# Performance work log

Measured on AMD Instinct MI355X. Metric: run time of the kernel, lower is better.

The kernel has to match this reference:

```python
import jax, jax.numpy as jnp
import numpy as np

SNUM = 8           # number of select-PUF stages
PUF_LEN = 64       # arbiter PUF length -> phi dim = PUF_LEN + 1
BATCH = 262144     # number of challenge-response pairs
D = 2 ** SNUM      # 256 combinations


def _make_kron_tables():
    """Replicates the W/B kron construction from combineMPUF.__init__.
    Returns Wmat, Bmat of shape [SNUM, D]; row i is W[i]/B[i] (originally [1, D])."""
    tmpX = np.array([[1], [1]])
    Ws, Bs = [], []
    for i in range(SNUM):
        w = np.array([[-1], [1]])
        b = np.array([[1], [0]])
        for _ in range(i + 1, SNUM):
            w = np.kron(tmpX, w)
            b = np.kron(tmpX, b)
        for _ in range(i):
            w = np.kron(w, tmpX)
            b = np.kron(b, tmpX)
        Ws.append(w.T[0])
        Bs.append(b.T[0])
    return (jnp.asarray(np.stack(Ws), jnp.float32),
            jnp.asarray(np.stack(Bs), jnp.float32))


def setup_inputs() -> dict:
    key = jax.random.key(0)
    k_phi, k_ws, k_bs, k_wd, k_bd = jax.random.split(key, 5)
    F = PUF_LEN + 1
    scale = 1.0 / np.sqrt(F)  # ~ torch Linear init scale
    phi = jax.random.normal(k_phi, (BATCH, F), dtype=jnp.float32)
    W_S = jax.random.uniform(k_ws, (SNUM, F), jnp.float32, -scale, scale)
    b_S = jax.random.uniform(k_bs, (SNUM,), jnp.float32, -scale, scale)
    W_D = jax.random.uniform(k_wd, (D, F), jnp.float32, -scale, scale)
    b_D = jax.random.uniform(k_bd, (D,), jnp.float32, -scale, scale)
    Wmat, Bmat = _make_kron_tables()
    return {"phi": phi, "W_S": W_S, "b_S": b_S, "W_D": W_D, "b_D": b_D,
            "Wmat": Wmat, "Bmat": Bmat}


def reference(phi, W_S, b_S, W_D, b_D, Wmat, Bmat):
    # phi: [B, F]; W_S: [SNUM, F]; W_D: [D, F]; Wmat/Bmat: [SNUM, D]
    Sdelta = phi @ W_S.T + b_S            # [B, SNUM]
    Ddelta = phi @ W_D.T + b_D            # [B, D]
    Souts = jax.nn.sigmoid(Sdelta)        # [B, SNUM]
    Douts = jax.nn.sigmoid(Ddelta)        # [B, D]
    # sigmoid-gated outer-product chain: M = prod_i (s_i * w_i + b_i)
    M = jnp.ones_like(Douts)
    for i in range(SNUM):                 # small fixed structural loop
        M = M * (Souts[:, i:i + 1] * Wmat[i] + Bmat[i])
    ans = jnp.sum(Douts * M * 0.99999, axis=-1, keepdims=True)  # [B, 1]
    reliability_output = jnp.abs(Sdelta)  # [B, SNUM]
    return ans, reliability_output
```

## Files before the change

### kernel.cpp

```cpp
#include <hip/hip_runtime.h>

typedef float  f32x4  __attribute__((ext_vector_type(4)));
typedef float  f32x4a __attribute__((ext_vector_type(4), aligned(4)));
typedef float  f32x2a __attribute__((ext_vector_type(2), aligned(4)));
typedef __bf16 bf16x8 __attribute__((ext_vector_type(8)));
typedef short  short8 __attribute__((ext_vector_type(8)));

#define F      65
#define NTT    17
#define KS3    3
#define RPB    128
#define NCHUNK (NTT*KS3*64)
#define NEGL2E -1.4426950408889634f

__device__ __forceinline__ float fast_sigmoid(float x) {
  float e = __builtin_amdgcn_exp2f(NEGL2E * x);
  return __builtin_amdgcn_rcpf(1.0f + e);
}
__device__ __forceinline__ float sig_prescaled(float a) {
  return __builtin_amdgcn_rcpf(1.0f + __builtin_amdgcn_exp2f(a));
}
template<int CTRL>
__device__ __forceinline__ float dpp_mov(float v) {
  return __builtin_bit_cast(float,
    __builtin_amdgcn_update_dpp(0, __builtin_bit_cast(int, v), CTRL, 0xF, 0xF, true));
}
__device__ __forceinline__ float reduce16(float v) {
  v += dpp_mov<0xB1>(v);
  v += dpp_mov<0x4E>(v);
  v += dpp_mov<0x141>(v);
  v += dpp_mov<0x140>(v);
  return v;
}

__global__ void prep_w(const float* __restrict__ W_S, const float* __restrict__ b_S,
                       const float* __restrict__ W_D, const float* __restrict__ b_D,
                       unsigned short* __restrict__ wsb) {
  int b = blockIdx.x;
  int t = b / 3, s = b % 3;
  int l = threadIdx.x;
  int c = l & 15, q = l >> 4;
  short8 out;
#pragma unroll
  for (int j = 0; j < 8; ++j) {
    int k = 32 * s + 8 * q + j;
    float v = 0.0f;
    if (t < 16) {
      int n = 16 * t + c;
      if (k < F)       v = NEGL2E * W_D[n * F + k];
      else if (k == F) v = NEGL2E * b_D[n];
    } else if (c < 8) {
      if (k < F)       v = W_S[c * F + k];
      else if (k == F) v = b_S[c];
    }
    unsigned int u = __builtin_bit_cast(unsigned int, v);
    u += 0x7FFFu + ((u >> 16) & 1u);
    out[j] = (short)(u >> 16);
  }
  reinterpret_cast<short8*>(wsb)[b * 64 + l] = out;
}

__launch_bounds__(256, 2)
__global__ void mpuf_main(const float* __restrict__ phi,
                          const unsigned short* __restrict__ wsb,
                          float* __restrict__ out_ans,
                          float* __restrict__ out_rel) {
  __shared__ short8 ldsB[NCHUNK];
  __shared__ float  soutv[RPB][9];
  __shared__ float  mtrec[RPB][20];

  const int tid  = threadIdx.x;
  const int wave = tid >> 6;
  const int l    = tid & 63;
  const int c    = l & 15;
  const int q    = l >> 4;
  const int wrow = wave * 32;
  const int brow = blockIdx.x * RPB;

  const float* prow0 = phi + (size_t)(brow + wrow + c) * F;
  const float* prow1 = prow0 + (size_t)16 * F;

  f32x4a f40[4], f41[4];
#pragma unroll
  for (int s = 0; s < 2; ++s) {
    f40[2 * s]     = *reinterpret_cast<const f32x4a*>(prow0 + 32 * s + 8 * q);
    f40[2 * s + 1] = *reinterpret_cast<const f32x4a*>(prow0 + 32 * s + 8 * q + 4);
    f41[2 * s]     = *reinterpret_cast<const f32x4a*>(prow1 + 32 * s + 8 * q);
    f41[2 * s + 1] = *reinterpret_cast<const f32x4a*>(prow1 + 32 * s + 8 * q + 4);
  }
  const float a640 = prow0[64];
  const float a641 = prow1[64];

  const short8* wsv = reinterpret_cast<const short8*>(wsb);
#pragma unroll
  for (int i = 0; i < 13; ++i) {
    int idx = tid + i * 256;
    if (idx < NCHUNK) ldsB[idx] = wsv[idx];
  }

  bf16x8 af0[3], af1[3];
#pragma unroll
  for (int s = 0; s < 2; ++s) {
    bf16x8 v0, v1;
#pragma unroll
    for (int j = 0; j < 4; ++j) {
      v0[j]     = (__bf16)f40[s * 2][j];
      v0[j + 4] = (__bf16)f40[s * 2 + 1][j];
      v1[j]     = (__bf16)f41[s * 2][j];
      v1[j + 4] = (__bf16)f41[s * 2 + 1][j];
    }
    af0[s] = v0; af1[s] = v1;
  }
  {
    bf16x8 v0 = {}, v1 = {};
    if (q == 0) {
      v0[0] = (__bf16)a640; v0[1] = (__bf16)1.0f;
      v1[0] = (__bf16)a641; v1[1] = (__bf16)1.0f;
    }
    af0[2] = v0; af1[2] = v1;
  }

  __syncthreads();

  f32x4 aS0 = {}, aS1 = {};
#pragma unroll
  for (int s = 0; s < KS3; ++s) {
    bf16x8 b = __builtin_bit_cast(bf16x8, ldsB[(16 * KS3 + s) * 64 + l]);
    aS0 = __builtin_amdgcn_mfma_f32_16x16x32_bf16(af0[s], b, aS0, 0, 0, 0);
    aS1 = __builtin_amdgcn_mfma_f32_16x16x32_bf16(af1[s], b, aS1, 0, 0, 0);
  }
  if (c < 8) {
#pragma unroll
    for (int r = 0; r < 4; ++r) {
      const int R0 = wrow + q * 4 + r, R1 = R0 + 16;
      out_rel[(size_t)(brow + R0) * 8 + c] = fabsf(aS0[r]);
      out_rel[(size_t)(brow + R1) * 8 + c] = fabsf(aS1[r]);
      soutv[R0][c] = fast_sigmoid(aS0[r]);
      soutv[R1][c] = fast_sigmoid(aS1[r]);
    }
  }

  float Ml0[4], Ml1[4];
#pragma unroll
  for (int rr = 0; rr < 8; ++rr) {
    const int R = wrow + (rr & 4) * 4 + q * 4 + (rr & 3);
    f32x2a p01 = *reinterpret_cast<const f32x2a*>(&soutv[R][0]);
    f32x2a p23 = *reinterpret_cast<const f32x2a*>(&soutv[R][2]);
    f32x2a p45 = *reinterpret_cast<const f32x2a*>(&soutv[R][4]);
    f32x2a p67 = *reinterpret_cast<const f32x2a*>(&soutv[R][6]);
    float m = 0.99999f;
    m *= (c & 1) ? p01[0] : 1.0f - p01[0];
    m *= (c & 2) ? p01[1] : 1.0f - p01[1];
    m *= (c & 4) ? p23[0] : 1.0f - p23[0];
    m *= (c & 8) ? p23[1] : 1.0f - p23[1];
    if (rr < 4) Ml0[rr & 3] = m; else Ml1[rr & 3] = m;
    float mt = (c & 1) ? p45[0] : 1.0f - p45[0];
    mt *= (c & 2) ? p45[1] : 1.0f - p45[1];
    mt *= (c & 4) ? p67[0] : 1.0f - p67[0];
    mt *= (c & 8) ? p67[1] : 1.0f - p67[1];
    mtrec[R][c] = mt;
  }

  float ans0[4] = {0, 0, 0, 0}, ans1[4] = {0, 0, 0, 0};

#pragma unroll
  for (int tp = 0; tp < 4; ++tp) {
    f32x4 w0[4], w1[4];
#pragma unroll
    for (int r = 0; r < 4; ++r) {
      const int R0 = wrow + q * 4 + r;
      w0[r] = *reinterpret_cast<const f32x4*>(&mtrec[R0][4 * tp]);
      w1[r] = *reinterpret_cast<const f32x4*>(&mtrec[R0 + 16][4 * tp]);
    }
#pragma unroll
    for (int tt = 0; tt < 4; ++tt) {
      const int t = 4 * tp + tt;
      f32x4 A0 = {}, A1 = {};
#pragma unroll
      for (int s = 0; s < KS3; ++s) {
        bf16x8 b = __builtin_bit_cast(bf16x8, ldsB[(t * KS3 + s) * 64 + l]);
        A0 = __builtin_amdgcn_mfma_f32_16x16x32_bf16(af0[s], b, A0, 0, 0, 0);
        A1 = __builtin_amdgcn_mfma_f32_16x16x32_bf16(af1[s], b, A1, 0, 0, 0);
      }
#pragma unroll
      for (int r = 0; r < 4; ++r) {
        ans0[r] = fmaf(sig_prescaled(A0[r]), w0[r][tt], ans0[r]);
        ans1[r] = fmaf(sig_prescaled(A1[r]), w1[r][tt], ans1[r]);
      }
    }
  }

#pragma unroll
  for (int r = 0; r < 4; ++r) {
    ans0[r] = reduce16(Ml0[r] * ans0[r]);
    ans1[r] = reduce16(Ml1[r] * ans1[r]);
  }
  if (c == 0) {
    f32x4 o0 = { ans0[0], ans0[1], ans0[2], ans0[3] };
    f32x4 o1 = { ans1[0], ans1[1], ans1[2], ans1[3] };
    *reinterpret_cast<f32x4*>(&out_ans[brow + wrow + q * 4])      = o0;
    *reinterpret_cast<f32x4*>(&out_ans[brow + wrow + 16 + q * 4]) = o1;
  }
}

extern "C" void kernel_launch(void* const* d_in, const int* in_sizes, int n_in,
                              void* d_out, int out_size, void* d_ws, size_t ws_size,
                              hipStream_t stream) {
  const float* phi = (const float*)d_in[0];
  const float* W_S = (const float*)d_in[1];
  const float* b_S = (const float*)d_in[2];
  const float* W_D = (const float*)d_in[3];
  const float* b_D = (const float*)d_in[4];
  const int rows = in_sizes[0] / F;
  unsigned short* wsb = (unsigned short*)d_ws;
  float* out_ans = (float*)d_out;
  float* out_rel = out_ans + rows;
  hipLaunchKernelGGL(prep_w, dim3(NTT * KS3), dim3(64), 0, stream,
                     W_S, b_S, W_D, b_D, wsb);
  hipLaunchKernelGGL(mpuf_main, dim3(rows / RPB), dim3(256), 0, stream,
                     phi, wsb, out_ans, out_rel);
}
```

Measured before the change: 44.78 us.

## Read weight fragments from global/L2 directly instead of staging in LDS

Drops the block-wide LDS staging of all bf16 weight chunks and the barrier after it. Each lane now loads its own B fragments straight from global memory (L2-resident) per tile. The LDS mtrec table is replaced by per-row register products of the upper four select sigmoids, and launch bounds go from 2 to 3 blocks per SM. This cuts LDS footprint and the sync stall, at the cost of more global load latency in the MFMA loop and higher register pressure.

```diff
diff --git a/kernel.cpp b/kernel.cpp
--- a/kernel.cpp
+++ b/kernel.cpp
@@ -2,7 +2,6 @@
 
 typedef float  f32x4  __attribute__((ext_vector_type(4)));
 typedef float  f32x4a __attribute__((ext_vector_type(4), aligned(4)));
-typedef float  f32x2a __attribute__((ext_vector_type(2), aligned(4)));
 typedef __bf16 bf16x8 __attribute__((ext_vector_type(8)));
 typedef short  short8 __attribute__((ext_vector_type(8)));
 
@@ -10,7 +9,6 @@
 #define NTT    17
 #define KS3    3
 #define RPB    128
-#define NCHUNK (NTT*KS3*64)
 #define NEGL2E -1.4426950408889634f
 
 __device__ __forceinline__ float fast_sigmoid(float x) {
@@ -60,14 +58,12 @@
   reinterpret_cast<short8*>(wsb)[b * 64 + l] = out;
 }
 
-__launch_bounds__(256, 2)
+__launch_bounds__(256, 3)
 __global__ void mpuf_main(const float* __restrict__ phi,
                           const unsigned short* __restrict__ wsb,
                           float* __restrict__ out_ans,
                           float* __restrict__ out_rel) {
-  __shared__ short8 ldsB[NCHUNK];
-  __shared__ float  soutv[RPB][9];
-  __shared__ float  mtrec[RPB][20];
+  __shared__ float soutv[RPB][12];
 
   const int tid  = threadIdx.x;
   const int wave = tid >> 6;
@@ -92,11 +88,9 @@
   const float a641 = prow1[64];
 
   const short8* wsv = reinterpret_cast<const short8*>(wsb);
-#pragma unroll
-  for (int i = 0; i < 13; ++i) {
-    int idx = tid + i * 256;
-    if (idx < NCHUNK) ldsB[idx] = wsv[idx];
-  }
+  short8 bS[3];
+#pragma unroll
+  for (int s = 0; s < 3; ++s) bS[s] = wsv[(16 * KS3 + s) * 64 + l];
 
   bf16x8 af0[3], af1[3];
 #pragma unroll
@@ -120,12 +114,10 @@
     af0[2] = v0; af1[2] = v1;
   }
 
-  __syncthreads();
-
   f32x4 aS0 = {}, aS1 = {};
 #pragma unroll
   for (int s = 0; s < KS3; ++s) {
-    bf16x8 b = __builtin_bit_cast(bf16x8, ldsB[(16 * KS3 + s) * 64 + l]);
+    bf16x8 b = __builtin_bit_cast(bf16x8, bS[s]);
     aS0 = __builtin_amdgcn_mfma_f32_16x16x32_bf16(af0[s], b, aS0, 0, 0, 0);
     aS1 = __builtin_amdgcn_mfma_f32_16x16x32_bf16(af1[s], b, aS1, 0, 0, 0);
   }
@@ -140,64 +132,57 @@
     }
   }
 
-  float Ml0[4], Ml1[4];
+  float Ml[8];
+  f32x4 a45[8], a67[8];
 #pragma unroll
   for (int rr = 0; rr < 8; ++rr) {
-    const int R = wrow + (rr & 4) * 4 + q * 4 + (rr & 3);
-    f32x2a p01 = *reinterpret_cast<const f32x2a*>(&soutv[R][0]);
-    f32x2a p23 = *reinterpret_cast<const f32x2a*>(&soutv[R][2]);
-    f32x2a p45 = *reinterpret_cast<const f32x2a*>(&soutv[R][4]);
-    f32x2a p67 = *reinterpret_cast<const f32x2a*>(&soutv[R][6]);
+    const int R = wrow + (rr >> 2) * 16 + q * 4 + (rr & 3);
+    f32x4 s03 = *reinterpret_cast<const f32x4*>(&soutv[R][0]);
+    f32x4 s47 = *reinterpret_cast<const f32x4*>(&soutv[R][4]);
     float m = 0.99999f;
-    m *= (c & 1) ? p01[0] : 1.0f - p01[0];
-    m *= (c & 2) ? p01[1] : 1.0f - p01[1];
-    m *= (c & 4) ? p23[0] : 1.0f - p23[0];
-    m *= (c & 8) ? p23[1] : 1.0f - p23[1];
-    if (rr < 4) Ml0[rr & 3] = m; else Ml1[rr & 3] = m;
-    float mt = (c & 1) ? p45[0] : 1.0f - p45[0];
-    mt *= (c & 2) ? p45[1] : 1.0f - p45[1];
-    mt *= (c & 4) ? p67[0] : 1.0f - p67[0];
-    mt *= (c & 8) ? p67[1] : 1.0f - p67[1];
-    mtrec[R][c] = mt;
-  }
-
-  float ans0[4] = {0, 0, 0, 0}, ans1[4] = {0, 0, 0, 0};
-
-#pragma unroll
-  for (int tp = 0; tp < 4; ++tp) {
-    f32x4 w0[4], w1[4];
+    m *= (c & 1) ? s03[0] : 1.0f - s03[0];
+    m *= (c & 2) ? s03[1] : 1.0f - s03[1];
+    m *= (c & 4) ? s03[2] : 1.0f - s03[2];
+    m *= (c & 8) ? s03[3] : 1.0f - s03[3];
+    Ml[rr] = m;
+    float o4 = 1.0f - s47[0], o5 = 1.0f - s47[1];
+    float o6 = 1.0f - s47[2], o7 = 1.0f - s47[3];
+    a45[rr] = f32x4{ o4 * o5, s47[0] * o5, o4 * s47[1], s47[0] * s47[1] };
+    a67[rr] = f32x4{ o6 * o7, s47[2] * o7, o6 * s47[3], s47[2] * s47[3] };
+  }
+
+  float ans[8];
+#pragma unroll
+  for (int rr = 0; rr < 8; ++rr) ans[rr] = 0.0f;
+
+#pragma unroll
+  for (int t = 0; t < 16; ++t) {
+    short8 bt[3];
+#pragma unroll
+    for (int s = 0; s < 3; ++s) bt[s] = wsv[(t * KS3 + s) * 64 + l];
+    f32x4 A0 = {}, A1 = {};
+#pragma unroll
+    for (int s = 0; s < KS3; ++s) {
+      bf16x8 b = __builtin_bit_cast(bf16x8, bt[s]);
+      A0 = __builtin_amdgcn_mfma_f32_16x16x32_bf16(af0[s], b, A0, 0, 0, 0);
+      A1 = __builtin_amdgcn_mfma_f32_16x16x32_bf16(af1[s], b, A1, 0, 0, 0);
+    }
 #pragma unroll
     for (int r = 0; r < 4; ++r) {
-      const int R0 = wrow + q * 4 + r;
-      w0[r] = *reinterpret_cast<const f32x4*>(&mtrec[R0][4 * tp]);
-      w1[r] = *reinterpret_cast<const f32x4*>(&mtrec[R0 + 16][4 * tp]);
-    }
-#pragma unroll
-    for (int tt = 0; tt < 4; ++tt) {
-      const int t = 4 * tp + tt;
-      f32x4 A0 = {}, A1 = {};
-#pragma unroll
-      for (int s = 0; s < KS3; ++s) {
-        bf16x8 b = __builtin_bit_cast(bf16x8, ldsB[(t * KS3 + s) * 64 + l]);
-        A0 = __builtin_amdgcn_mfma_f32_16x16x32_bf16(af0[s], b, A0, 0, 0, 0);
-        A1 = __builtin_amdgcn_mfma_f32_16x16x32_bf16(af1[s], b, A1, 0, 0, 0);
-      }
-#pragma unroll
-      for (int r = 0; r < 4; ++r) {
-        ans0[r] = fmaf(sig_prescaled(A0[r]), w0[r][tt], ans0[r]);
-        ans1[r] = fmaf(sig_prescaled(A1[r]), w1[r][tt], ans1[r]);
-      }
-    }
-  }
-
+      float mt0 = a45[r][t & 3] * a67[r][t >> 2];
+      float mt1 = a45[4 + r][t & 3] * a67[4 + r][t >> 2];
+      ans[r]     = fmaf(sig_prescaled(A0[r]), mt0, ans[r]);
+      ans[4 + r] = fmaf(sig_prescaled(A1[r]), mt1, ans[4 + r]);
+    }
+  }
+
+  f32x4 o0, o1;
 #pragma unroll
   for (int r = 0; r < 4; ++r) {
-    ans0[r] = reduce16(Ml0[r] * ans0[r]);
-    ans1[r] = reduce16(Ml1[r] * ans1[r]);
+    o0[r] = reduce16(Ml[r] * ans[r]);
+    o1[r] = reduce16(Ml[4 + r] * ans[4 + r]);
   }
   if (c == 0) {
-    f32x4 o0 = { ans0[0], ans0[1], ans0[2], ans0[3] };
-    f32x4 o1 = { ans1[0], ans1[1], ans1[2], ans1[3] };
     *reinterpret_cast<f32x4*>(&out_ans[brow + wrow + q * 4])      = o0;
     *reinterpret_cast<f32x4*>(&out_ans[brow + wrow + 16 + q * 4]) = o1;
   }
```

New measurement: 70.62 us. +57.7%, slower.
